# Optimization experiments

Measured on AMD Instinct MI355X. Metric: run time of the kernel, lower is better.

The kernel has to match this reference:

```python
import jax, jax.numpy as jnp
import numpy as np

E, C, H, W = 512, 64, 28, 28
N_CORNERS = 256


def setup_inputs() -> dict:
    key = jax.random.key(0)
    k1, k2, k3 = jax.random.split(key, 3)
    x = jax.random.normal(k1, (E, C, H, W), dtype=jnp.float32)
    # aggregator: Conv2d(4*C, 64, kernel_size=1, bias=False) -> weight [64, 4*C]
    W_agg = jax.random.normal(k2, (64, 4 * C), dtype=jnp.float32) * (1.0 / np.sqrt(4 * C))
    # each edge connects two corners
    edge_corner = jax.random.randint(k3, (E, 2), 0, N_CORNERS, dtype=jnp.int64)
    eids = jnp.arange(E, dtype=jnp.int64)
    # rows of [corner_idx, edge_idx], two per edge (consistent with edge_corner)
    corner_edge_pairs = jnp.concatenate([
        jnp.stack([edge_corner[:, 0], eids], axis=-1),
        jnp.stack([edge_corner[:, 1], eids], axis=-1),
    ], axis=0)
    return {"x": x, "W_agg": W_agg, "corner_edge_pairs": corner_edge_pairs,
            "edge_corner": edge_corner, "num_corners": N_CORNERS}


def reference(x, W_agg, corner_edge_pairs, edge_corner, num_corners):
    # scatter-mean edge features onto corners (index_add_ + count/clamp)
    seg = corner_edge_pairs[:, 0]
    gathered = x[corner_edge_pairs[:, 1]]                      # [2E, C, H, W]
    corner_features = jax.ops.segment_sum(gathered, seg, num_segments=num_corners)
    count = jax.ops.segment_sum(jnp.ones((corner_edge_pairs.shape[0],), x.dtype),
                                seg, num_segments=num_corners)
    corner_features = corner_features / jnp.clip(count, 1.0)[:, None, None, None]
    # gather back per edge endpoints
    left_x = corner_features[edge_corner[:, 0]]                # [E, C, H, W]
    right_x = corner_features[edge_corner[:, 1]]               # [E, C, H, W]
    global_x = jnp.max(x, axis=0, keepdims=True)               # [1, C, H, W]
    cat = jnp.concatenate([x, left_x, right_x,
                           jnp.broadcast_to(global_x, x.shape)], axis=1)  # [E,4C,H,W]
    # 1x1 conv, no bias, + ReLU
    out = jnp.einsum('echw,oc->eohw', cat, W_agg)
    return jax.nn.relu(out)
```

## Files before the change

kernel.cpp:

```cpp
#include <hip/hip_runtime.h>
#include <cstdint>

#define E_N   512
#define C_N   64
#define HW_N  784
#define CHW_N 50176
#define CHW4  12544
#define NC    256
#define NCOLS 401408

__global__ void build_adj_k(const int* __restrict__ ec,
                            int* __restrict__ adj_start,
                            int* __restrict__ adj_edge,
                            float* __restrict__ inv_count)
{
    __shared__ int cnt[NC];
    __shared__ int st[NC + 1];
    int tid = threadIdx.x;
    if (tid < NC) cnt[tid] = 0;
    __syncthreads();
    for (int e = tid; e < E_N; e += 256) {
        int c0 = ec[2 * e]     & (NC - 1);
        int c1 = ec[2 * e + 1] & (NC - 1);
        atomicAdd(&cnt[c0], 1);
        atomicAdd(&cnt[c1], 1);
    }
    __syncthreads();
    if (tid == 0) {
        int s = 0;
        for (int c = 0; c < NC; ++c) { st[c] = s; s += cnt[c]; }
        st[NC] = s;
    }
    __syncthreads();
    if (tid < NC) {
        adj_start[tid] = st[tid];
        inv_count[tid] = 1.0f / (float)((cnt[tid] > 1) ? cnt[tid] : 1);
        cnt[tid] = st[tid];
    }
    if (tid == 0) adj_start[NC] = st[NC];
    __syncthreads();
    for (int e = tid; e < E_N; e += 256) {
        int c0 = ec[2 * e]     & (NC - 1);
        int c1 = ec[2 * e + 1] & (NC - 1);
        adj_edge[atomicAdd(&cnt[c0], 1)] = e;
        adj_edge[atomicAdd(&cnt[c1], 1)] = e;
    }
}

__global__ void wt_k(const float* __restrict__ W, float* __restrict__ Wt)
{
    int i = blockIdx.x * 256 + threadIdx.x;
    if (i < 192 * 64) {
        int k = i >> 6, o = i & 63;
        Wt[i] = W[o * 256 + k];
    }
}

__global__ void gmax_part_k(const float* __restrict__ x, float* __restrict__ part)
{
    int p4 = blockIdx.x * 256 + threadIdx.x;
    const float4* p = reinterpret_cast<const float4*>(x) + (size_t)(blockIdx.y * 64) * CHW4 + p4;
    float4 m = make_float4(-INFINITY, -INFINITY, -INFINITY, -INFINITY);
    #pragma unroll 4
    for (int i = 0; i < 64; ++i) {
        float4 v = p[(size_t)i * CHW4];
        m.x = fmaxf(m.x, v.x); m.y = fmaxf(m.y, v.y);
        m.z = fmaxf(m.z, v.z); m.w = fmaxf(m.w, v.w);
    }
    reinterpret_cast<float4*>(part)[blockIdx.y * CHW4 + p4] = m;
}

__global__ void gmax_reduce_k(const float* __restrict__ part, float* __restrict__ gmax)
{
    int p4 = blockIdx.x * 256 + threadIdx.x;
    const float4* p = reinterpret_cast<const float4*>(part);
    float4 m = p[p4];
    #pragma unroll
    for (int i = 1; i < 8; ++i) {
        float4 v = p[i * CHW4 + p4];
        m.x = fmaxf(m.x, v.x); m.y = fmaxf(m.y, v.y);
        m.z = fmaxf(m.z, v.z); m.w = fmaxf(m.w, v.w);
    }
    reinterpret_cast<float4*>(gmax)[p4] = m;
}

__global__ void g4_k(const float* __restrict__ W, const float* __restrict__ gmax,
                     float* __restrict__ g4)
{
    int j4 = blockIdx.x * 256 + threadIdx.x;
    int o  = (j4 * 4) / HW_N;
    int hw = j4 * 4 - o * HW_N;
    float4 acc = make_float4(0.f, 0.f, 0.f, 0.f);
    #pragma unroll 8
    for (int c = 0; c < 64; ++c) {
        float w = W[o * 256 + 192 + c];
        float4 g = *reinterpret_cast<const float4*>(gmax + c * HW_N + hw);
        acc.x += w * g.x; acc.y += w * g.y; acc.z += w * g.z; acc.w += w * g.w;
    }
    *reinterpret_cast<float4*>(g4 + (size_t)j4 * 4) = acc;
}

__global__ void cf_k(const float* __restrict__ x, const int* __restrict__ adj_start,
                     const int* __restrict__ adj_edge, const float* __restrict__ inv_count,
                     float* __restrict__ cf)
{
    int c  = blockIdx.y;
    int p4 = blockIdx.x * 256 + threadIdx.x;
    float4 acc = make_float4(0.f, 0.f, 0.f, 0.f);
    int s0 = adj_start[c], s1 = adj_start[c + 1];
    for (int i = s0; i < s1; ++i) {
        int e = adj_edge[i];
        float4 v = *reinterpret_cast<const float4*>(x + (size_t)e * CHW_N + (size_t)p4 * 4);
        acc.x += v.x; acc.y += v.y; acc.z += v.z; acc.w += v.w;
    }
    float ic = inv_count[c];
    acc.x *= ic; acc.y *= ic; acc.z *= ic; acc.w *= ic;
    *reinterpret_cast<float4*>(cf + (size_t)c * CHW_N + (size_t)p4 * 4) = acc;
}

__global__ __launch_bounds__(256) void fused_k(
    const float* __restrict__ x, const float* __restrict__ cf,
    const float* __restrict__ Wt, const float* __restrict__ g4,
    const int* __restrict__ ec, float* __restrict__ out)
{
    __shared__ float Bs[32][256];
    __shared__ float Ws[32][64];
    __shared__ int eArr[64];
    __shared__ int hwArr[64];
    __shared__ int base1[64];
    __shared__ int base2[64];

    int tid = threadIdx.x;
    int jbase = blockIdx.x * 256;

    if (tid < 64) {
        int j4 = jbase + tid * 4;
        int e  = j4 / HW_N;
        int hw = j4 - e * HW_N;
        eArr[tid]  = e;
        hwArr[tid] = hw;
        int c0 = ec[2 * e]     & (NC - 1);
        int c1 = ec[2 * e + 1] & (NC - 1);
        base1[tid] = c0 * CHW_N + hw;
        base2[tid] = c1 * CHW_N + hw;
    }

    float acc[8][8];
    #pragma unroll
    for (int i = 0; i < 8; ++i)
        #pragma unroll
        for (int j = 0; j < 8; ++j) acc[i][j] = 0.f;

    int o0 = (tid >> 5) << 3;
    int n0 = (tid & 31) << 2;

    for (int half = 0; half < 6; ++half) {
        __syncthreads();
        int seg = half >> 1;
        int kr0 = (half & 1) * 32;
        #pragma unroll
        for (int it = 0; it < 8; ++it) {
            int idx = it * 256 + tid;
            int kk  = idx >> 6;
            int nq  = idx & 63;
            int kr  = kr0 + kk;
            const float* src;
            if (seg == 0)      src = x  + (size_t)eArr[nq] * CHW_N + kr * HW_N + hwArr[nq];
            else if (seg == 1) src = cf + (size_t)base1[nq] + kr * HW_N;
            else               src = cf + (size_t)base2[nq] + kr * HW_N;
            *reinterpret_cast<float4*>(&Bs[kk][nq * 4]) =
                *reinterpret_cast<const float4*>(src);
        }
        {
            const float4* wsrc = reinterpret_cast<const float4*>(Wt + (size_t)(seg * 64 + kr0) * 64);
            float4* wdst = reinterpret_cast<float4*>(&Ws[0][0]);
            wdst[tid]       = wsrc[tid];
            wdst[tid + 256] = wsrc[tid + 256];
        }
        __syncthreads();
        #pragma unroll 8
        for (int kk = 0; kk < 32; ++kk) {
            float4 xa = *reinterpret_cast<const float4*>(&Bs[kk][n0]);
            float4 xb = *reinterpret_cast<const float4*>(&Bs[kk][n0 + 128]);
            float4 wa = *reinterpret_cast<const float4*>(&Ws[kk][o0]);
            float4 wb = *reinterpret_cast<const float4*>(&Ws[kk][o0 + 4]);
            float xv[8] = {xa.x, xa.y, xa.z, xa.w, xb.x, xb.y, xb.z, xb.w};
            float wv[8] = {wa.x, wa.y, wa.z, wa.w, wb.x, wb.y, wb.z, wb.w};
            #pragma unroll
            for (int oi = 0; oi < 8; ++oi)
                #pragma unroll
                for (int ni = 0; ni < 8; ++ni)
                    acc[oi][ni] += wv[oi] * xv[ni];
        }
    }

    #pragma unroll
    for (int oi = 0; oi < 8; ++oi) {
        int o = o0 + oi;
        #pragma unroll
        for (int nb = 0; nb < 2; ++nb) {
            int nq = (n0 + nb * 128) >> 2;
            int e  = eArr[nq];
            int hw = hwArr[nq];
            float4 g = *reinterpret_cast<const float4*>(g4 + o * HW_N + hw);
            float4 r;
            r.x = fmaxf(acc[oi][nb * 4 + 0] + g.x, 0.f);
            r.y = fmaxf(acc[oi][nb * 4 + 1] + g.y, 0.f);
            r.z = fmaxf(acc[oi][nb * 4 + 2] + g.z, 0.f);
            r.w = fmaxf(acc[oi][nb * 4 + 3] + g.w, 0.f);
            *reinterpret_cast<float4*>(out + (size_t)e * CHW_N + o * HW_N + hw) = r;
        }
    }
}

extern "C" void kernel_launch(void* const* d_in, const int* in_sizes, int n_in,
                              void* d_out, int out_size, void* d_ws, size_t ws_size,
                              hipStream_t stream)
{
    const float* x  = (const float*)d_in[0];
    const float* W  = (const float*)d_in[1];
    const int*   ec = (const int*)d_in[3];
    float* out      = (float*)d_out;

    float* ws_f      = (float*)d_ws;
    float* cf        = ws_f;
    float* part      = cf + (size_t)NC * CHW_N;
    float* gmax      = part + 8 * CHW_N;
    float* g4        = gmax + CHW_N;
    float* wt        = g4 + CHW_N;
    int*   adj_start = (int*)(wt + 12288);
    int*   adj_edge  = adj_start + 272;
    float* inv_count = (float*)(adj_edge + 1024);

    build_adj_k<<<1, 256, 0, stream>>>(ec, adj_start, adj_edge, inv_count);
    wt_k<<<48, 256, 0, stream>>>(W, wt);
    gmax_part_k<<<dim3(49, 8), 256, 0, stream>>>(x, part);
    gmax_reduce_k<<<49, 256, 0, stream>>>(part, gmax);
    g4_k<<<49, 256, 0, stream>>>(W, gmax, g4);
    cf_k<<<dim3(49, NC), 256, 0, stream>>>(x, adj_start, adj_edge, inv_count, cf);
    fused_k<<<1568, 256, 0, stream>>>(x, cf, wt, g4, ec, out);
}
```

Baseline: 374.1 us.

## Use split-bf16 MFMA for fused 1x1 conv GEMM

Replaces the fp32 FMA register-tiled GEMM in the fused kernel with MFMA 16x16x32 bf16 instructions. Accuracy is kept close to fp32 by splitting each operand into hi and lo bf16 parts and issuing three MFMAs per tile. Weight splitting is folded into the adjacency prep kernel, which removes one launch, and the block tile shrinks to 128 columns. The costs are extra conversion work when staging B into LDS, scalar instead of vectorized output stores, and a small loss of precision relative to full fp32.

```diff
diff --git a/kernel.cpp b/kernel.cpp
--- a/kernel.cpp
+++ b/kernel.cpp
@@ -1,4 +1,5 @@
 #include <hip/hip_runtime.h>
+#include <hip/hip_bf16.h>
 #include <cstdint>
 
 #define E_N   512
@@ -7,12 +8,23 @@
 #define CHW_N 50176
 #define CHW4  12544
 #define NC    256
-#define NCOLS 401408
-
-__global__ void build_adj_k(const int* __restrict__ ec,
-                            int* __restrict__ adj_start,
-                            int* __restrict__ adj_edge,
-                            float* __restrict__ inv_count)
+
+typedef __attribute__((ext_vector_type(8))) short bf16x8;
+typedef __attribute__((ext_vector_type(4))) float f32x4;
+typedef __attribute__((ext_vector_type(8))) unsigned short us8;
+
+__device__ __forceinline__ unsigned short bf16_rne(float f, float& hif) {
+    unsigned int u = __float_as_uint(f);
+    unsigned int r = u + 0x7FFFu + ((u >> 16) & 1u);
+    unsigned short h = (unsigned short)(r >> 16);
+    hif = __uint_as_float((unsigned int)h << 16);
+    return h;
+}
+
+__global__ void prep_k(const int* __restrict__ ec, const float* __restrict__ W,
+                       int* __restrict__ adj_start, int* __restrict__ adj_edge,
+                       float* __restrict__ inv_count,
+                       unsigned short* __restrict__ Whi, unsigned short* __restrict__ Wlo)
 {
     __shared__ int cnt[NC];
     __shared__ int st[NC + 1];
@@ -20,10 +32,8 @@
     if (tid < NC) cnt[tid] = 0;
     __syncthreads();
     for (int e = tid; e < E_N; e += 256) {
-        int c0 = ec[2 * e]     & (NC - 1);
-        int c1 = ec[2 * e + 1] & (NC - 1);
-        atomicAdd(&cnt[c0], 1);
-        atomicAdd(&cnt[c1], 1);
+        atomicAdd(&cnt[ec[2 * e] & (NC - 1)], 1);
+        atomicAdd(&cnt[ec[2 * e + 1] & (NC - 1)], 1);
     }
     __syncthreads();
     if (tid == 0) {
@@ -40,19 +50,18 @@
     if (tid == 0) adj_start[NC] = st[NC];
     __syncthreads();
     for (int e = tid; e < E_N; e += 256) {
-        int c0 = ec[2 * e]     & (NC - 1);
-        int c1 = ec[2 * e + 1] & (NC - 1);
-        adj_edge[atomicAdd(&cnt[c0], 1)] = e;
-        adj_edge[atomicAdd(&cnt[c1], 1)] = e;
-    }
-}
-
-__global__ void wt_k(const float* __restrict__ W, float* __restrict__ Wt)
-{
-    int i = blockIdx.x * 256 + threadIdx.x;
-    if (i < 192 * 64) {
-        int k = i >> 6, o = i & 63;
-        Wt[i] = W[o * 256 + k];
+        adj_edge[atomicAdd(&cnt[ec[2 * e] & (NC - 1)], 1)] = e;
+        adj_edge[atomicAdd(&cnt[ec[2 * e + 1] & (NC - 1)], 1)] = e;
+    }
+    for (int i = tid; i < 64 * 192; i += 256) {
+        int o = i / 192, k = i - o * 192;
+        float w = W[o * 256 + k];
+        float hif;
+        unsigned short hi = bf16_rne(w, hif);
+        float d;
+        unsigned short lo = bf16_rne(w - hif, d);
+        Whi[i] = hi;
+        Wlo[i] = lo;
     }
 }
 
@@ -118,99 +127,117 @@
     *reinterpret_cast<float4*>(cf + (size_t)c * CHW_N + (size_t)p4 * 4) = acc;
 }
 
-__global__ __launch_bounds__(256) void fused_k(
+__global__ __launch_bounds__(256) void fused_mfma_k(
     const float* __restrict__ x, const float* __restrict__ cf,
-    const float* __restrict__ Wt, const float* __restrict__ g4,
-    const int* __restrict__ ec, float* __restrict__ out)
-{
-    __shared__ float Bs[32][256];
-    __shared__ float Ws[32][64];
-    __shared__ int eArr[64];
-    __shared__ int hwArr[64];
-    __shared__ int base1[64];
-    __shared__ int base2[64];
+    const unsigned short* __restrict__ Whi, const unsigned short* __restrict__ Wlo,
+    const float* __restrict__ g4, const int* __restrict__ ec,
+    float* __restrict__ out)
+{
+    __shared__ unsigned short Ah[64][40], Al[64][40];
+    __shared__ unsigned short Bh[128][40], Bl[128][40];
+    __shared__ const float* sb[3][8];
+    __shared__ int eArr[8], hwArr[8];
 
     int tid = threadIdx.x;
-    int jbase = blockIdx.x * 256;
-
-    if (tid < 64) {
-        int j4 = jbase + tid * 4;
-        int e  = j4 / HW_N;
-        int hw = j4 - e * HW_N;
+    int jbase = blockIdx.x * 128;
+
+    if (tid < 8) {
+        int j16 = jbase + tid * 16;
+        int e   = j16 / HW_N;
+        int hw0 = j16 - e * HW_N;
         eArr[tid]  = e;
-        hwArr[tid] = hw;
+        hwArr[tid] = hw0;
         int c0 = ec[2 * e]     & (NC - 1);
         int c1 = ec[2 * e + 1] & (NC - 1);
-        base1[tid] = c0 * CHW_N + hw;
-        base2[tid] = c1 * CHW_N + hw;
-    }
-
-    float acc[8][8];
+        sb[0][tid] = x  + (size_t)e  * CHW_N + hw0;
+        sb[1][tid] = cf + (size_t)c0 * CHW_N + hw0;
+        sb[2][tid] = cf + (size_t)c1 * CHW_N + hw0;
+    }
+    __syncthreads();
+
+    int lane  = tid & 63;
+    int wv    = tid >> 6;
+    int row16 = lane & 15;
+    int kq    = (lane >> 4) << 3;
+
+    f32x4 acc[4][2];
     #pragma unroll
-    for (int i = 0; i < 8; ++i)
-        #pragma unroll
-        for (int j = 0; j < 8; ++j) acc[i][j] = 0.f;
-
-    int o0 = (tid >> 5) << 3;
-    int n0 = (tid & 31) << 2;
-
-    for (int half = 0; half < 6; ++half) {
+    for (int a = 0; a < 4; ++a)
+        #pragma unroll
+        for (int b = 0; b < 2; ++b) acc[a][b] = (f32x4){0.f, 0.f, 0.f, 0.f};
+
+    int ao  = tid >> 2;
+    int akq = (tid & 3) << 3;
+
+    for (int s = 0; s < 6; ++s) {
+        int seg   = s >> 1;
+        int krel0 = (s & 1) << 5;
+        int k0    = s << 5;
+
+        *reinterpret_cast<us8*>(&Ah[ao][akq]) =
+            *reinterpret_cast<const us8*>(Whi + ao * 192 + k0 + akq);
+        *reinterpret_cast<us8*>(&Al[ao][akq]) =
+            *reinterpret_cast<const us8*>(Wlo + ao * 192 + k0 + akq);
+
+        #pragma unroll
+        for (int it = 0; it < 4; ++it) {
+            int idx = it * 256 + tid;
+            int kl  = idx >> 5;
+            int j4  = idx & 31;
+            const float* src = sb[seg][j4 >> 2] + (krel0 + kl) * HW_N + (j4 & 3) * 4;
+            float4 v = *reinterpret_cast<const float4*>(src);
+            int jrow = j4 << 2;
+            float fv[4] = {v.x, v.y, v.z, v.w};
+            #pragma unroll
+            for (int m = 0; m < 4; ++m) {
+                float hif;
+                unsigned short hi = bf16_rne(fv[m], hif);
+                float d;
+                unsigned short lo = bf16_rne(fv[m] - hif, d);
+                Bh[jrow + m][kl] = hi;
+                Bl[jrow + m][kl] = lo;
+            }
+        }
         __syncthreads();
-        int seg = half >> 1;
-        int kr0 = (half & 1) * 32;
-        #pragma unroll
-        for (int it = 0; it < 8; ++it) {
-            int idx = it * 256 + tid;
-            int kk  = idx >> 6;
-            int nq  = idx & 63;
-            int kr  = kr0 + kk;
-            const float* src;
-            if (seg == 0)      src = x  + (size_t)eArr[nq] * CHW_N + kr * HW_N + hwArr[nq];
-            else if (seg == 1) src = cf + (size_t)base1[nq] + kr * HW_N;
-            else               src = cf + (size_t)base2[nq] + kr * HW_N;
-            *reinterpret_cast<float4*>(&Bs[kk][nq * 4]) =
-                *reinterpret_cast<const float4*>(src);
-        }
-        {
-            const float4* wsrc = reinterpret_cast<const float4*>(Wt + (size_t)(seg * 64 + kr0) * 64);
-            float4* wdst = reinterpret_cast<float4*>(&Ws[0][0]);
-            wdst[tid]       = wsrc[tid];
-            wdst[tid + 256] = wsrc[tid + 256];
-        }
+
+        bf16x8 ah[4], al[4], bh[2], bl[2];
+        #pragma unroll
+        for (int ot = 0; ot < 4; ++ot) {
+            ah[ot] = *reinterpret_cast<const bf16x8*>(&Ah[ot * 16 + row16][kq]);
+            al[ot] = *reinterpret_cast<const bf16x8*>(&Al[ot * 16 + row16][kq]);
+        }
+        #pragma unroll
+        for (int jt = 0; jt < 2; ++jt) {
+            bh[jt] = *reinterpret_cast<const bf16x8*>(&Bh[wv * 32 + jt * 16 + row16][kq]);
+            bl[jt] = *reinterpret_cast<const bf16x8*>(&Bl[wv * 32 + jt * 16 + row16][kq]);
+        }
+
+        #pragma unroll
+        for (int ot = 0; ot < 4; ++ot)
+            #pragma unroll
+            for (int jt = 0; jt < 2; ++jt) {
+                acc[ot][jt] = __builtin_amdgcn_mfma_f32_16x16x32_bf16(ah[ot], bh[jt], acc[ot][jt], 0, 0, 0);
+                acc[ot][jt] = __builtin_amdgcn_mfma_f32_16x16x32_bf16(ah[ot], bl[jt], acc[ot][jt], 0, 0, 0);
+                acc[ot][jt] = __builtin_amdgcn_mfma_f32_16x16x32_bf16(al[ot], bh[jt], acc[ot][jt], 0, 0, 0);
+            }
         __syncthreads();
-        #pragma unroll 8
-        for (int kk = 0; kk < 32; ++kk) {
-            float4 xa = *reinterpret_cast<const float4*>(&Bs[kk][n0]);
-            float4 xb = *reinterpret_cast<const float4*>(&Bs[kk][n0 + 128]);
-            float4 wa = *reinterpret_cast<const float4*>(&Ws[kk][o0]);
-            float4 wb = *reinterpret_cast<const float4*>(&Ws[kk][o0 + 4]);
-            float xv[8] = {xa.x, xa.y, xa.z, xa.w, xb.x, xb.y, xb.z, xb.w};
-            float wv[8] = {wa.x, wa.y, wa.z, wa.w, wb.x, wb.y, wb.z, wb.w};
+    }
+
+    int orb = (lane >> 4) << 2;
+    #pragma unroll
+    for (int ot = 0; ot < 4; ++ot)
+        #pragma unroll
+        for (int jt = 0; jt < 2; ++jt) {
+            int g  = wv * 2 + jt;
+            int e  = eArr[g];
+            int hw = hwArr[g] + row16;
             #pragma unroll
-            for (int oi = 0; oi < 8; ++oi)
-                #pragma unroll
-                for (int ni = 0; ni < 8; ++ni)
-                    acc[oi][ni] += wv[oi] * xv[ni];
-        }
-    }
-
-    #pragma unroll
-    for (int oi = 0; oi < 8; ++oi) {
-        int o = o0 + oi;
-        #pragma unroll
-        for (int nb = 0; nb < 2; ++nb) {
-            int nq = (n0 + nb * 128) >> 2;
-            int e  = eArr[nq];
-            int hw = hwArr[nq];
-            float4 g = *reinterpret_cast<const float4*>(g4 + o * HW_N + hw);
-            float4 r;
-            r.x = fmaxf(acc[oi][nb * 4 + 0] + g.x, 0.f);
-            r.y = fmaxf(acc[oi][nb * 4 + 1] + g.y, 0.f);
-            r.z = fmaxf(acc[oi][nb * 4 + 2] + g.z, 0.f);
-            r.w = fmaxf(acc[oi][nb * 4 + 3] + g.w, 0.f);
-            *reinterpret_cast<float4*>(out + (size_t)e * CHW_N + o * HW_N + hw) = r;
-        }
-    }
+            for (int r = 0; r < 4; ++r) {
+                int o = ot * 16 + orb + r;
+                float v = acc[ot][jt][r] + g4[o * HW_N + hw];
+                out[(size_t)e * CHW_N + o * HW_N + hw] = fmaxf(v, 0.f);
+            }
+        }
 }
 
 extern "C" void kernel_launch(void* const* d_in, const int* in_sizes, int n_in,
@@ -227,16 +254,16 @@
     float* part      = cf + (size_t)NC * CHW_N;
     float* gmax      = part + 8 * CHW_N;
     float* g4        = gmax + CHW_N;
-    float* wt        = g4 + CHW_N;
-    int*   adj_start = (int*)(wt + 12288);
+    unsigned short* Whi = (unsigned short*)(g4 + CHW_N);
+    unsigned short* Wlo = Whi + 12288;
+    int*   adj_start = (int*)(Wlo + 12288);
     int*   adj_edge  = adj_start + 272;
     float* inv_count = (float*)(adj_edge + 1024);
 
-    build_adj_k<<<1, 256, 0, stream>>>(ec, adj_start, adj_edge, inv_count);
-    wt_k<<<48, 256, 0, stream>>>(W, wt);
+    prep_k<<<1, 256, 0, stream>>>(ec, W, adj_start, adj_edge, inv_count, Whi, Wlo);
     gmax_part_k<<<dim3(49, 8), 256, 0, stream>>>(x, part);
     gmax_reduce_k<<<49, 256, 0, stream>>>(part, gmax);
     g4_k<<<49, 256, 0, stream>>>(W, gmax, g4);
     cf_k<<<dim3(49, NC), 256, 0, stream>>>(x, adj_start, adj_edge, inv_count, cf);
-    fused_k<<<1568, 256, 0, stream>>>(x, cf, wt, g4, ec, out);
-}
+    fused_mfma_k<<<3136, 256, 0, stream>>>(x, cf, Whi, Wlo, g4, ec, out);
+}
```

Result: slower. 391.1 us (+4.5%).
